# Performance work log

Hardware: AMD Instinct MI355X
Metric: run time of the kernel (lower is better)

The kernel has to match this reference:

```python
import jax, jax.numpy as jnp
import numpy as np

B, L, H, X = 64, 512, 1024, 1024
D = H + X  # 2048


def setup_inputs() -> dict:
    key = jax.random.key(0)
    k = jax.random.split(key, 8)
    h_state = jax.random.normal(k[0], (B, L, H), dtype=jnp.float32)
    x = jax.random.normal(k[1], (B, L, X), dtype=jnp.float32)
    trigger = jax.random.randint(k[2], (B, 1), 0, L, dtype=jnp.int64)
    mask = jax.random.randint(k[3], (B, L), 0, 2, dtype=jnp.int32)
    # Linear params (torch Linear: y = x @ W.T + b)
    sa = 1.0 / np.sqrt(D)
    ss = 1.0 / np.sqrt(H)
    W_a = jax.random.uniform(k[4], (D, D), jnp.float32, -sa, sa)
    b_a = jax.random.uniform(k[5], (D,), jnp.float32, -sa, sa)
    W_s = jax.random.uniform(k[6], (D, H), jnp.float32, -ss, ss)
    b_s = jax.random.uniform(k[7], (D,), jnp.float32, -ss, ss)
    return {"h_state": h_state, "x": x, "W_a": W_a, "b_a": b_a,
            "W_s": W_s, "b_s": b_s, "trigger": trigger, "mask": mask}


def reference(h_state, x, W_a, b_a, W_s, b_s, trigger, mask):
    # a: [B, L, D]
    a = jnp.concatenate((h_state, x), axis=-1)
    # direct gather of the trigger position (replaces one_hot+masked_select)
    trig_a = jnp.take_along_axis(a, trigger[:, :, None], axis=1)  # [B, 1, D]
    s = h_state.sum(axis=1)  # [B, H]
    et = jnp.tanh(jnp.einsum('bld,ed->ble', a, W_a) + b_a
                  + (s @ W_s.T + b_s)[:, None, :])  # [B, L, D]
    et = jnp.where(mask[:, :, None] == 0, jnp.float32(-1e9), et)
    attn = jax.nn.softmax(et, axis=-1)  # softmax over feature dim D (as in source)
    # dropout is identity in eval mode
    out = (trig_a * attn).sum(axis=1)  # [B, D]
    return out
```

## Files before the change

### kernel.cpp

```cpp
#include <hip/hip_runtime.h>
#include <cstdint>

#define B_ 64
#define L_ 512
#define H_ 1024
#define D_ 2048

typedef __attribute__((ext_vector_type(8))) short short8;
typedef __attribute__((ext_vector_type(4))) float f32x4;
typedef unsigned int u32;

static __device__ __forceinline__ float bf2f(u32 lo16) {
    u32 u = lo16 << 16;
    return __builtin_bit_cast(float, u);
}
static __device__ __forceinline__ unsigned short f2bf(float f) {
    u32 u = __builtin_bit_cast(u32, f);
    u += 0x7fffu + ((u >> 16) & 1u);
    return (unsigned short)(u >> 16);
}
static __device__ __forceinline__ u32 pk(float x, float y) {
    return (u32)f2bf(x) | ((u32)f2bf(y) << 16);
}
static __device__ __forceinline__ float fast_pexp(float u) {
    u = fminf(15.f, fmaxf(-15.f, u));
    float ex = __expf(2.f * u);
    float th = (ex - 1.f) / (ex + 1.f);
    return __expf(th);
}
static __device__ __forceinline__ void gload_lds16(const unsigned short* g, unsigned short* l) {
    __builtin_amdgcn_global_load_lds((const __attribute__((address_space(1))) u32*)g,
                                     (__attribute__((address_space(3))) u32*)l, 16, 0, 0);
}

__global__ __launch_bounds__(256) void k_s(const float* __restrict__ h, float* __restrict__ s) {
    int t = blockIdx.x * 256 + threadIdx.x;
    int b = t >> 10, hh = t & 1023;
    const float* p = h + ((size_t)b * L_) * H_ + hh;
    float acc = 0.f;
#pragma unroll 8
    for (int l = 0; l < L_; ++l) acc += p[(size_t)l * H_];
    s[t] = acc;
}

__global__ __launch_bounds__(256) void k_compact(const int* __restrict__ mask,
                                                 const float* __restrict__ ba,
                                                 const float* __restrict__ bs,
                                                 int* __restrict__ ridx,
                                                 int* __restrict__ cnt1,
                                                 float* __restrict__ cnt0,
                                                 float* __restrict__ t2) {
    int b = blockIdx.x;
    __shared__ int sm[L_];
    for (int l = threadIdx.x; l < L_; l += 256) sm[l] = mask[b * L_ + l];
    for (int e = threadIdx.x; e < D_; e += 256) t2[b * D_ + e] = ba[e] + bs[e];
    __syncthreads();
    if (threadIdx.x == 0) {
        int* rb = ridx + b * L_;
        int c = 0;
        for (int l = 0; l < L_; ++l) if (sm[l]) rb[c++] = l;
        int n1 = c;
        int last = (c > 0) ? rb[c - 1] : 0;
        for (; c < L_; ++c) rb[c] = last;
        cnt1[b] = n1;
        cnt0[b] = (float)(L_ - n1);
    }
}

__global__ __launch_bounds__(256) void k_cvtW(const float* __restrict__ Wa,
                                              unsigned short* __restrict__ Wb) {
    int t = blockIdx.x * 256 + threadIdx.x;
    float4 v = ((const float4*)Wa)[t];
    ((uint2*)Wb)[t] = make_uint2(pk(v.x, v.y), pk(v.z, v.w));
}

__global__ __launch_bounds__(256) void k_prep(const float* __restrict__ hs, const float* __restrict__ xx,
                                              const int* __restrict__ ridx, const int* __restrict__ cnt1,
                                              unsigned short* __restrict__ Abf) {
    int j = blockIdx.x;
    int b = blockIdx.y;
    int n1 = cnt1[b];
    if (j >= ((n1 + 127) & ~127)) return;
    int l = ridx[b * L_ + j];
    int t = threadIdx.x;
    size_t rb = ((size_t)(b * L_ + l)) << 10;
    const float* src = (t < 128) ? (hs + rb + t * 8) : (xx + rb + (t - 128) * 8);
    float4 v0 = *(const float4*)src;
    float4 v1 = *(const float4*)(src + 4);
    *(uint4*)(Abf + (((size_t)(b * L_ + j)) << 11) + t * 8) =
        make_uint4(pk(v0.x, v0.y), pk(v0.z, v0.w), pk(v1.x, v1.y), pk(v1.z, v1.w));
}

__global__ __launch_bounds__(256) void k_t2(const float* __restrict__ s, const float* __restrict__ Ws,
                                            float* __restrict__ t2) {
    __shared__ float As[16][64];
    __shared__ float Bs[16][64];
    int n0 = blockIdx.x * 64;
    int ks0 = blockIdx.y * 256;
    int tid = threadIdx.x;
    int tx = tid & 15, ty = tid >> 4;
    int r = tid >> 2, q = tid & 3;
    float acc[4][4] = {};
    for (int k0 = ks0; k0 < ks0 + 256; k0 += 16) {
        float4 av = *(const float4*)(s + (size_t)r * H_ + k0 + q * 4);
        float4 bv = *(const float4*)(Ws + (size_t)(n0 + r) * H_ + k0 + q * 4);
        __syncthreads();
        As[q*4+0][r] = av.x; As[q*4+1][r] = av.y; As[q*4+2][r] = av.z; As[q*4+3][r] = av.w;
        Bs[q*4+0][r] = bv.x; Bs[q*4+1][r] = bv.y; Bs[q*4+2][r] = bv.z; Bs[q*4+3][r] = bv.w;
        __syncthreads();
#pragma unroll
        for (int kk = 0; kk < 16; ++kk) {
            float a_[4], b_[4];
            *(float4*)&a_[0] = *(const float4*)&As[kk][ty * 4];
            *(float4*)&b_[0] = *(const float4*)&Bs[kk][tx * 4];
#pragma unroll
            for (int i = 0; i < 4; ++i)
#pragma unroll
                for (int j = 0; j < 4; ++j) acc[i][j] += a_[i] * b_[j];
        }
    }
#pragma unroll
    for (int i = 0; i < 4; ++i)
#pragma unroll
        for (int j = 0; j < 4; ++j)
            atomicAdd(&t2[(size_t)(ty * 4 + i) * D_ + n0 + tx * 4 + j], acc[i][j]);
}

#define BM 128
#define BN 128
#define BK 32

__global__ __launch_bounds__(256) void k_gemm2(
    const unsigned short* __restrict__ Abf, const unsigned short* __restrict__ Wb,
    const float* __restrict__ t2, const int* __restrict__ cnt1,
    float* __restrict__ rowsum, unsigned short* __restrict__ P)
{
    __shared__ unsigned short Asl[BM * BK];
    __shared__ unsigned short Bsl[BN * BK];
    __shared__ float red[BM];

    int tid = threadIdx.x;
    int lane = tid & 63;
    int w = tid >> 6;
    int wm = w & 1, wn = w >> 1;

    int n0 = blockIdx.x * BN;
    int jt = blockIdx.y;
    int b = jt >> 2;
    int j0 = (jt & 3) * BM;
    int n1 = cnt1[b];
    if (j0 >= n1) return;

    const unsigned short* ga = Abf + (((size_t)(b * L_ + j0 + w * 32 + (lane >> 2))) << 11) + (lane & 3) * 8;
    const unsigned short* gb = Wb  + (((size_t)(n0 + w * 32 + (lane >> 2))) << 11) + (lane & 3) * 8;
    unsigned short* la = &Asl[w * 1024];
    unsigned short* lb = &Bsl[w * 1024];

    int cl = lane & 15, kb = (lane >> 4) * 8;
    f32x4 acc[4][4] = {};

    for (int k0 = 0; k0 < D_; k0 += BK) {
        __syncthreads();
        gload_lds16(ga + k0,         la);
        gload_lds16(ga + 32768 + k0, la + 512);
        gload_lds16(gb + k0,         lb);
        gload_lds16(gb + 32768 + k0, lb + 512);
        __syncthreads();
        short8 af[4], bfg[4];
#pragma unroll
        for (int i = 0; i < 4; ++i) af[i]  = *(const short8*)&Asl[(wm*64 + i*16 + cl) * BK + kb];
#pragma unroll
        for (int j = 0; j < 4; ++j) bfg[j] = *(const short8*)&Bsl[(wn*64 + j*16 + cl) * BK + kb];
#pragma unroll
        for (int i = 0; i < 4; ++i)
#pragma unroll
            for (int j = 0; j < 4; ++j)
                acc[i][j] = __builtin_amdgcn_mfma_f32_16x16x32_bf16(af[i], bfg[j], acc[i][j], 0, 0, 0);
    }

    int qd = lane >> 4;
    float t2v[4]; int ecol[4];
#pragma unroll
    for (int j = 0; j < 4; ++j) { ecol[j] = n0 + wn*64 + j*16 + cl; t2v[j] = t2[b * D_ + ecol[j]]; }
    int orow0 = b * L_ + j0;

    float rs[4][4] = {};
#pragma unroll
    for (int i = 0; i < 4; ++i) {
        int lrowb = wm*64 + i*16 + qd*4;
#pragma unroll
        for (int j = 0; j < 4; ++j) {
#pragma unroll
            for (int g = 0; g < 4; ++g) {
                float p = fast_pexp(acc[i][j][g] + t2v[j]);
                rs[i][g] += p;
                P[(size_t)(orow0 + lrowb + g) * D_ + ecol[j]] = f2bf(p);
            }
        }
    }
#pragma unroll
    for (int i = 0; i < 4; ++i)
#pragma unroll
        for (int g = 0; g < 4; ++g) {
            float v = rs[i][g];
            v += __shfl_xor(v, 1); v += __shfl_xor(v, 2);
            v += __shfl_xor(v, 4); v += __shfl_xor(v, 8);
            rs[i][g] = v;
        }
    __syncthreads();
    if (tid < BM) red[tid] = 0.f;
    __syncthreads();
    if (cl == 0) {
#pragma unroll
        for (int i = 0; i < 4; ++i)
#pragma unroll
            for (int g = 0; g < 4; ++g)
                atomicAdd(&red[wm*64 + i*16 + qd*4 + g], rs[i][g]);
    }
    __syncthreads();
    if (tid < BM) atomicAdd(&rowsum[orow0 + tid], red[tid]);
}

__global__ __launch_bounds__(256) void k_fin2(const unsigned short* __restrict__ P,
                                              const float* __restrict__ rowsum,
                                              const int* __restrict__ cnt1,
                                              const int* __restrict__ trigger,
                                              const float* __restrict__ hs,
                                              const float* __restrict__ xx,
                                              float* __restrict__ out) {
    int b = blockIdx.y;
    __shared__ float iv[L_];
    int n1 = cnt1[b];
    int lceil = (n1 + 127) & ~127;
    for (int j = threadIdx.x; j < L_; j += 256)
        iv[j] = (j < n1) ? 1.f / rowsum[b * L_ + j] : 0.f;
    __syncthreads();
    int e0 = blockIdx.x * 512 + threadIdx.x * 2;
    const unsigned short* Pb = P + (((size_t)b) << 20) + e0;
    float s0 = 0.f, s1 = 0.f;
#pragma unroll 8
    for (int l = 0; l < lceil; ++l) {
        float f = iv[l];
        u32 pv = *(const u32*)(Pb + (((size_t)l) << 11));
        s0 += f * bf2f(pv & 0xffffu);
        s1 += f * bf2f(pv >> 16);
    }
    float base = (float)(L_ - n1) * (1.f / 2048.f);
    int trig = trigger[b];
    size_t tb = ((size_t)(b * L_ + trig)) << 10;
    float ta0 = (e0 < 1024) ? hs[tb + e0] : xx[tb + e0 - 1024];
    float ta1 = (e0 + 1 < 1024) ? hs[tb + e0 + 1] : xx[tb + e0 + 1 - 1024];
    out[b * D_ + e0]     = (s0 + base) * ta0;
    out[b * D_ + e0 + 1] = (s1 + base) * ta1;
}

#define LDK 40
__global__ __launch_bounds__(256) void k_gemm(
    const float* __restrict__ hs, const float* __restrict__ xx,
    const float* __restrict__ Wa, const unsigned short* __restrict__ Wb,
    const float* __restrict__ t2,
    const int* __restrict__ ridx, const int* __restrict__ cnt1,
    float* __restrict__ rowsum,
    unsigned short* __restrict__ P, float* __restrict__ out, int mode)
{
    __shared__ unsigned short Asl[BM][LDK];
    __shared__ unsigned short Bsl[BN][BK];
    __shared__ float red[BM];

    int tid = threadIdx.x;
    int lane = tid & 63;
    int w = tid >> 6;
    int wm = w & 1, wn = w >> 1;

    int n0 = blockIdx.x * BN;
    int jt = blockIdx.y;
    int b = jt >> 2;
    int j0 = (jt & 3) * BM;
    int n1 = cnt1[b];
    if (j0 >= n1) return;

    int r = tid >> 1;
    int koff = (tid & 1) * 16;
    int l = ridx[b * L_ + j0 + r];
    size_t abase = ((size_t)b * L_ + l) * (size_t)H_;
    const float* hrow = hs + abase;
    const float* xrow = xx + abase;
    const float* browf = Wa + (size_t)(n0 + r) * D_;
    const unsigned short* bw0 = Wb ? Wb + (size_t)(n0 + (tid >> 2)) * D_ + (tid & 3) * 8 : nullptr;
    const unsigned short* bw1 = Wb ? Wb + (size_t)(n0 + 64 + (tid >> 2)) * D_ + (tid & 3) * 8 : nullptr;
    unsigned short* bs0 = &Bsl[0][0] + (size_t)tid * 8;
    unsigned short* bs1 = &Bsl[0][0] + (size_t)(tid + 256) * 8;
    bool useWb = (Wb != nullptr);

    f32x4 acc[4][4] = {};

    for (int k0 = 0; k0 < D_; k0 += BK) {
        int k = k0 + koff;
        const float* ap = (k < H_) ? (hrow + k) : (xrow + (k - H_));
        float4 a0 = *(const float4*)(ap);
        float4 a1 = *(const float4*)(ap + 4);
        float4 a2 = *(const float4*)(ap + 8);
        float4 a3 = *(const float4*)(ap + 12);
        uint4 bv0, bv1;
        float4 c0, c1, c2, c3;
        if (useWb) {
            bv0 = *(const uint4*)(bw0 + k0);
            bv1 = *(const uint4*)(bw1 + k0);
        } else {
            const float* bp = browf + k;
            c0 = *(const float4*)(bp);
            c1 = *(const float4*)(bp + 4);
            c2 = *(const float4*)(bp + 8);
            c3 = *(const float4*)(bp + 12);
        }
        __syncthreads();
        *(uint4*)&Asl[r][koff]     = make_uint4(pk(a0.x,a0.y), pk(a0.z,a0.w), pk(a1.x,a1.y), pk(a1.z,a1.w));
        *(uint4*)&Asl[r][koff + 8] = make_uint4(pk(a2.x,a2.y), pk(a2.z,a2.w), pk(a3.x,a3.y), pk(a3.z,a3.w));
        if (useWb) {
            *(uint4*)bs0 = bv0;
            *(uint4*)bs1 = bv1;
        } else {
            *(uint4*)&Bsl[r][koff]     = make_uint4(pk(c0.x,c0.y), pk(c0.z,c0.w), pk(c1.x,c1.y), pk(c1.z,c1.w));
            *(uint4*)&Bsl[r][koff + 8] = make_uint4(pk(c2.x,c2.y), pk(c2.z,c2.w), pk(c3.x,c3.y), pk(c3.z,c3.w));
        }
        __syncthreads();
        int kb = (lane >> 4) * 8;
        short8 af[4], bfg[4];
#pragma unroll
        for (int i = 0; i < 4; ++i) af[i]  = *(const short8*)&Asl[wm*64 + i*16 + (lane & 15)][kb];
#pragma unroll
        for (int j = 0; j < 4; ++j) bfg[j] = *(const short8*)&Bsl[wn*64 + j*16 + (lane & 15)][kb];
#pragma unroll
        for (int i = 0; i < 4; ++i)
#pragma unroll
            for (int j = 0; j < 4; ++j)
                acc[i][j] = __builtin_amdgcn_mfma_f32_16x16x32_bf16(af[i], bfg[j], acc[i][j], 0, 0, 0);
    }

    int cl = lane & 15, qd = lane >> 4;
    float t2v[4]; int ecol[4];
#pragma unroll
    for (int j = 0; j < 4; ++j) { ecol[j] = n0 + wn*64 + j*16 + cl; t2v[j] = t2[b * D_ + ecol[j]]; }
    int orow0 = b * L_ + j0;

    if (mode <= 1) {
        float rs[4][4] = {};
#pragma unroll
        for (int i = 0; i < 4; ++i) {
            int lrowb = wm*64 + i*16 + qd*4;
#pragma unroll
            for (int j = 0; j < 4; ++j) {
#pragma unroll
                for (int g = 0; g < 4; ++g) {
                    float p = fast_pexp(acc[i][j][g] + t2v[j]);
                    rs[i][g] += p;
                    if (mode == 0)
                        P[(size_t)(orow0 + lrowb + g) * D_ + ecol[j]] = f2bf(p);
                }
            }
        }
#pragma unroll
        for (int i = 0; i < 4; ++i)
#pragma unroll
            for (int g = 0; g < 4; ++g) {
                float v = rs[i][g];
                v += __shfl_xor(v, 1); v += __shfl_xor(v, 2);
                v += __shfl_xor(v, 4); v += __shfl_xor(v, 8);
                rs[i][g] = v;
            }
        __syncthreads();
        if (tid < BM) red[tid] = 0.f;
        __syncthreads();
        if (cl == 0) {
#pragma unroll
            for (int i = 0; i < 4; ++i)
#pragma unroll
                for (int g = 0; g < 4; ++g)
                    atomicAdd(&red[wm*64 + i*16 + qd*4 + g], rs[i][g]);
        }
        __syncthreads();
        if (tid < BM) atomicAdd(&rowsum[orow0 + tid], red[tid]);
    } else {
        float inv[4][4];
#pragma unroll
        for (int i = 0; i < 4; ++i)
#pragma unroll
            for (int g = 0; g < 4; ++g) {
                int lrow = wm*64 + i*16 + qd*4 + g;
                inv[i][g] = (j0 + lrow < n1) ? (1.f / rowsum[orow0 + lrow]) : 0.f;
            }
        float cs[4] = {};
#pragma unroll
        for (int i = 0; i < 4; ++i)
#pragma unroll
            for (int j = 0; j < 4; ++j)
#pragma unroll
                for (int g = 0; g < 4; ++g)
                    cs[j] += fast_pexp(acc[i][j][g] + t2v[j]) * inv[i][g];
#pragma unroll
        for (int j = 0; j < 4; ++j) {
            float v = cs[j];
            v += __shfl_xor(v, 16); v += __shfl_xor(v, 32);
            cs[j] = v;
        }
        __syncthreads();
        if (tid < BN) red[tid] = 0.f;
        __syncthreads();
        if (qd == 0) {
#pragma unroll
            for (int j = 0; j < 4; ++j) atomicAdd(&red[wn*64 + j*16 + cl], cs[j]);
        }
        __syncthreads();
        if (tid < BN) atomicAdd(&out[b * D_ + n0 + tid], red[tid]);
    }
}

__global__ __launch_bounds__(256) void k_inv(const int* __restrict__ cnt1,
                                             const float* __restrict__ rowsum,
                                             float* __restrict__ invr) {
    int t = blockIdx.x * 256 + threadIdx.x;
    int b = t >> 9, j = t & 511;
    invr[t] = (j < cnt1[b]) ? (1.f / rowsum[t]) : 0.f;
}

__global__ __launch_bounds__(256) void k_fin(const unsigned short* __restrict__ P,
                                             const float* __restrict__ invr,
                                             const int* __restrict__ cnt1,
                                             float* __restrict__ out) {
    int b = blockIdx.y;
    int lz = blockIdx.z * 128;
    if (lz >= cnt1[b]) return;
    int e0 = blockIdx.x * 512 + threadIdx.x * 2;
    const unsigned short* Pb = P + ((size_t)b * L_ + lz) * D_ + e0;
    const float* ivb = invr + b * L_ + lz;
    float s0 = 0.f, s1 = 0.f;
    for (int l = 0; l < 128; ++l) {
        float iv = ivb[l];
        u32 pv = *(const u32*)(Pb + (size_t)l * D_);
        s0 += iv * bf2f(pv & 0xffffu);
        s1 += iv * bf2f(pv >> 16);
    }
    atomicAdd(&out[b * D_ + e0], s0);
    atomicAdd(&out[b * D_ + e0 + 1], s1);
}

__global__ __launch_bounds__(256) void k_final(
    const float* __restrict__ hs, const float* __restrict__ xx,
    const int* __restrict__ trigger, const float* __restrict__ cnt0,
    float* __restrict__ out) {
    int t = blockIdx.x * 256 + threadIdx.x;
    int b = t >> 11, e = t & 2047;
    int trig = trigger[b];
    size_t base = ((size_t)b * L_ + trig) * 1024;
    float ta = (e < 1024) ? hs[base + e] : xx[base + e - 1024];
    out[t] = (out[t] + cnt0[b] * (1.0f / 2048.0f)) * ta;
}

extern "C" void kernel_launch(void* const* d_in, const int* in_sizes, int n_in,
                              void* d_out, int out_size, void* d_ws, size_t ws_size,
                              hipStream_t stream) {
    const float* hs = (const float*)d_in[0];
    const float* xx = (const float*)d_in[1];
    const float* Wa = (const float*)d_in[2];
    const float* ba = (const float*)d_in[3];
    const float* Ws = (const float*)d_in[4];
    const float* bs = (const float*)d_in[5];
    const int*   trig = (const int*)d_in[6];
    const int*   mask = (const int*)d_in[7];
    float* out = (float*)d_out;

    float* wsf    = (float*)d_ws;
    float* s      = wsf;
    float* t2     = s + 65536;
    float* cnt0   = t2 + 131072;
    float* rowsum = cnt0 + 64;
    float* invr   = rowsum + 32768;
    int*   cnt1   = (int*)(invr + 32768);
    int*   ridx   = cnt1 + 64;
    unsigned short* P   = (unsigned short*)(ridx + 32768);
    unsigned short* Wb  = P + (size_t)B_ * L_ * D_;
    unsigned short* Abf = Wb + (size_t)D_ * D_;

    const size_t BASE_B   = 1180160ull;
    const size_t NEED_P   = BASE_B + 134217728ull;
    const size_t NEED_WB  = NEED_P + 8388608ull;
    const size_t NEED_ALL = NEED_WB + 134217728ull;
    bool haveP   = ws_size >= NEED_P;
    bool haveWb  = ws_size >= NEED_WB;
    bool haveAll = ws_size >= NEED_ALL;

    (void)hipMemsetAsync(rowsum, 0, (size_t)B_ * L_ * sizeof(float), stream);

    k_s      <<<256, 256, 0, stream>>>(hs, s);
    k_compact<<<B_, 256, 0, stream>>>(mask, ba, bs, ridx, cnt1, cnt0, t2);
    k_t2     <<<dim3(32, 4), 256, 0, stream>>>(s, Ws, t2);

    dim3 grid(D_ / BN, (B_ * L_) / BM);

    if (haveAll) {
        k_cvtW <<<4096, 256, 0, stream>>>(Wa, Wb);
        k_prep <<<dim3(512, 64), 256, 0, stream>>>(hs, xx, ridx, cnt1, Abf);
        k_gemm2<<<grid, 256, 0, stream>>>(Abf, Wb, t2, cnt1, rowsum, P);
        k_fin2 <<<dim3(4, 64), 256, 0, stream>>>(P, rowsum, cnt1, trig, hs, xx, out);
    } else {
        const unsigned short* WbArg = haveWb ? Wb : nullptr;
        if (haveWb) k_cvtW<<<4096, 256, 0, stream>>>(Wa, Wb);
        (void)hipMemsetAsync(out, 0, (size_t)B_ * D_ * sizeof(float), stream);
        if (haveP) {
            k_gemm<<<grid, 256, 0, stream>>>(hs, xx, Wa, WbArg, t2, ridx, cnt1, rowsum, P, out, 0);
            k_inv <<<(B_ * L_) / 256, 256, 0, stream>>>(cnt1, rowsum, invr);
            k_fin <<<dim3(4, 64, 4), 256, 0, stream>>>(P, invr, cnt1, out);
        } else {
            k_gemm<<<grid, 256, 0, stream>>>(hs, xx, Wa, WbArg, t2, ridx, cnt1, rowsum, P, out, 1);
            k_gemm<<<grid, 256, 0, stream>>>(hs, xx, Wa, WbArg, t2, ridx, cnt1, rowsum, P, out, 2);
        }
        k_final<<<(B_ * D_) / 256, 256, 0, stream>>>(hs, xx, trig, cnt0, out);
    }
}
```

Before: 680.2 us.

## Replace bf16 GEMM with 256x256-tile, 8-wave, double-buffered LDS pipelined kernel

Replaces the 128x128 single-buffered MFMA GEMM with a 256x256 tile kernel using 512 threads, a 64-wide K step and double-buffered LDS (128 KB). Global-to-LDS loads for the next K tiles are interleaved with four MFMA phases, using barriers and s_setprio to overlap memory traffic with matrix compute and to raise reuse per loaded byte. Row padding in the prep kernel moves to multiples of 256 to match the larger M tile. The larger tile wastes more work on partially masked batches and its heavy LDS and register use limits occupancy.

```diff
diff --git a/kernel.cpp b/kernel.cpp
--- a/kernel.cpp
+++ b/kernel.cpp
@@ -80,7 +80,7 @@
     int j = blockIdx.x;
     int b = blockIdx.y;
     int n1 = cnt1[b];
-    if (j >= ((n1 + 127) & ~127)) return;
+    if (j >= ((n1 + 255) & ~255)) return;
     int l = ridx[b * L_ + j];
     int t = threadIdx.x;
     size_t rb = ((size_t)(b * L_ + l)) << 10;
@@ -126,99 +126,183 @@
             atomicAdd(&t2[(size_t)(ty * 4 + i) * D_ + n0 + tx * 4 + j], acc[i][j]);
 }
 
-#define BM 128
-#define BN 128
-#define BK 32
-
-__global__ __launch_bounds__(256) void k_gemm2(
+#define BAR3() do { asm volatile("" ::: "memory"); __builtin_amdgcn_s_barrier(); asm volatile("" ::: "memory"); } while (0)
+
+__global__ __launch_bounds__(512, 2) void k_gemm3(
     const unsigned short* __restrict__ Abf, const unsigned short* __restrict__ Wb,
     const float* __restrict__ t2, const int* __restrict__ cnt1,
     float* __restrict__ rowsum, unsigned short* __restrict__ P)
 {
-    __shared__ unsigned short Asl[BM * BK];
-    __shared__ unsigned short Bsl[BN * BK];
-    __shared__ float red[BM];
+    __shared__ unsigned short lds[65536];
 
     int tid = threadIdx.x;
     int lane = tid & 63;
     int w = tid >> 6;
-    int wm = w & 1, wn = w >> 1;
-
-    int n0 = blockIdx.x * BN;
+    int wm = w >> 2;
+    int wn = w & 3;
+    int g = lane >> 4;
+    int cl = lane & 15;
+
+    int n0 = blockIdx.x * 256;
     int jt = blockIdx.y;
-    int b = jt >> 2;
-    int j0 = (jt & 3) * BM;
+    int b = jt >> 1;
+    int j0 = (jt & 1) * 256;
     int n1 = cnt1[b];
     if (j0 >= n1) return;
 
-    const unsigned short* ga = Abf + (((size_t)(b * L_ + j0 + w * 32 + (lane >> 2))) << 11) + (lane & 3) * 8;
-    const unsigned short* gb = Wb  + (((size_t)(n0 + w * 32 + (lane >> 2))) << 11) + (lane & 3) * 8;
-    unsigned short* la = &Asl[w * 1024];
-    unsigned short* lb = &Bsl[w * 1024];
-
-    int cl = lane & 15, kb = (lane >> 4) * 8;
-    f32x4 acc[4][4] = {};
-
-    for (int k0 = 0; k0 < D_; k0 += BK) {
-        __syncthreads();
-        gload_lds16(ga + k0,         la);
-        gload_lds16(ga + 32768 + k0, la + 512);
-        gload_lds16(gb + k0,         lb);
-        gload_lds16(gb + 32768 + k0, lb + 512);
-        __syncthreads();
-        short8 af[4], bfg[4];
-#pragma unroll
-        for (int i = 0; i < 4; ++i) af[i]  = *(const short8*)&Asl[(wm*64 + i*16 + cl) * BK + kb];
-#pragma unroll
-        for (int j = 0; j < 4; ++j) bfg[j] = *(const short8*)&Bsl[(wn*64 + j*16 + cl) * BK + kb];
-#pragma unroll
-        for (int i = 0; i < 4; ++i)
-#pragma unroll
-            for (int j = 0; j < 4; ++j)
-                acc[i][j] = __builtin_amdgcn_mfma_f32_16x16x32_bf16(af[i], bfg[j], acc[i][j], 0, 0, 0);
-    }
-
-    int qd = lane >> 4;
+    int sr = tid >> 2;
+    int sce = (tid & 3) * 8;
+    const unsigned short* aS0 = Abf + (((size_t)(b * L_ + j0 + sr)) << 11) + sce;
+    const unsigned short* aS1 = aS0 + ((size_t)128 << 11);
+    const unsigned short* bS0 = Wb + (((size_t)(n0 + sr)) << 11) + sce;
+    const unsigned short* bS1 = bS0 + ((size_t)128 << 11);
+    int wq = w * 512;
+
+#define STAGE_A3(h, tk, u) do { \
+        const unsigned short* s_ = ((h) ? aS1 : aS0) + (tk) * 64; \
+        unsigned short* d_ = &lds[(u) * 32768 + (h) * 8192 + wq]; \
+        gload_lds16(s_, d_); gload_lds16(s_ + 32, d_ + 4096); } while (0)
+#define STAGE_B3(h, tk, u) do { \
+        const unsigned short* s_ = ((h) ? bS1 : bS0) + (tk) * 64; \
+        unsigned short* d_ = &lds[(u) * 32768 + 16384 + (h) * 8192 + wq]; \
+        gload_lds16(s_, d_); gload_lds16(s_ + 32, d_ + 4096); } while (0)
+
+    int rdA = wm * 8192 + cl * 32 + g * 8;
+    int rdB = 16384 + (wn >> 1) * 8192 + ((wn & 1) * 64 + cl) * 32 + g * 8;
+
+    f32x4 acc[8][4] = {};
+    short8 af[4][2], bf0[2][2], bf1[2][2];
+
+    STAGE_A3(0, 0, 0); STAGE_B3(0, 0, 0); STAGE_B3(1, 0, 0); STAGE_A3(1, 0, 0);
+    STAGE_B3(0, 1, 1); STAGE_B3(1, 1, 1); STAGE_A3(0, 1, 1);
+    asm volatile("s_waitcnt vmcnt(6)" ::: "memory");
+    BAR3();
+
+    for (int t = 0; t < 32; ++t) {
+        int u = t & 1;
+        int ub = u * 32768;
+        int tn = (t + 1) & 31, tnn = (t + 2) & 31;
+
+#pragma unroll
+        for (int m = 0; m < 4; ++m) {
+            af[m][0] = *(const short8*)&lds[ub + rdA + m * 512];
+            af[m][1] = *(const short8*)&lds[ub + rdA + 4096 + m * 512];
+        }
+#pragma unroll
+        for (int n = 0; n < 2; ++n) {
+            bf0[n][0] = *(const short8*)&lds[ub + rdB + n * 512];
+            bf0[n][1] = *(const short8*)&lds[ub + rdB + 4096 + n * 512];
+        }
+        STAGE_A3(1, tn, u ^ 1);
+        BAR3();
+        __builtin_amdgcn_s_setprio(1);
+#pragma unroll
+        for (int m = 0; m < 4; ++m)
+#pragma unroll
+            for (int n = 0; n < 2; ++n) {
+                acc[m][n] = __builtin_amdgcn_mfma_f32_16x16x32_bf16(af[m][0], bf0[n][0], acc[m][n], 0, 0, 0);
+                acc[m][n] = __builtin_amdgcn_mfma_f32_16x16x32_bf16(af[m][1], bf0[n][1], acc[m][n], 0, 0, 0);
+            }
+        __builtin_amdgcn_s_setprio(0);
+        BAR3();
+
+#pragma unroll
+        for (int n = 0; n < 2; ++n) {
+            bf1[n][0] = *(const short8*)&lds[ub + rdB + (n + 2) * 512];
+            bf1[n][1] = *(const short8*)&lds[ub + rdB + 4096 + (n + 2) * 512];
+        }
+        BAR3();
+        __builtin_amdgcn_s_setprio(1);
+#pragma unroll
+        for (int m = 0; m < 4; ++m)
+#pragma unroll
+            for (int n = 0; n < 2; ++n) {
+                acc[m][n + 2] = __builtin_amdgcn_mfma_f32_16x16x32_bf16(af[m][0], bf1[n][0], acc[m][n + 2], 0, 0, 0);
+                acc[m][n + 2] = __builtin_amdgcn_mfma_f32_16x16x32_bf16(af[m][1], bf1[n][1], acc[m][n + 2], 0, 0, 0);
+            }
+        __builtin_amdgcn_s_setprio(0);
+        BAR3();
+
+#pragma unroll
+        for (int m = 0; m < 4; ++m) {
+            af[m][0] = *(const short8*)&lds[ub + rdA + (m + 4) * 512];
+            af[m][1] = *(const short8*)&lds[ub + rdA + 4096 + (m + 4) * 512];
+        }
+        STAGE_B3(0, tnn, u);
+        BAR3();
+        __builtin_amdgcn_s_setprio(1);
+#pragma unroll
+        for (int m = 0; m < 4; ++m)
+#pragma unroll
+            for (int n = 0; n < 2; ++n) {
+                acc[m + 4][n + 2] = __builtin_amdgcn_mfma_f32_16x16x32_bf16(af[m][0], bf1[n][0], acc[m + 4][n + 2], 0, 0, 0);
+                acc[m + 4][n + 2] = __builtin_amdgcn_mfma_f32_16x16x32_bf16(af[m][1], bf1[n][1], acc[m + 4][n + 2], 0, 0, 0);
+            }
+        __builtin_amdgcn_s_setprio(0);
+        BAR3();
+
+        STAGE_B3(1, tnn, u);
+        STAGE_A3(0, tnn, u);
+        asm volatile("s_waitcnt vmcnt(6)" ::: "memory");
+        BAR3();
+        __builtin_amdgcn_s_setprio(1);
+#pragma unroll
+        for (int m = 0; m < 4; ++m)
+#pragma unroll
+            for (int n = 0; n < 2; ++n) {
+                acc[m + 4][n] = __builtin_amdgcn_mfma_f32_16x16x32_bf16(af[m][0], bf0[n][0], acc[m + 4][n], 0, 0, 0);
+                acc[m + 4][n] = __builtin_amdgcn_mfma_f32_16x16x32_bf16(af[m][1], bf0[n][1], acc[m + 4][n], 0, 0, 0);
+            }
+        __builtin_amdgcn_s_setprio(0);
+        BAR3();
+    }
+#undef STAGE_A3
+#undef STAGE_B3
+
+    asm volatile("s_waitcnt vmcnt(0)" ::: "memory");
+    __syncthreads();
+
     float t2v[4]; int ecol[4];
 #pragma unroll
-    for (int j = 0; j < 4; ++j) { ecol[j] = n0 + wn*64 + j*16 + cl; t2v[j] = t2[b * D_ + ecol[j]]; }
-    int orow0 = b * L_ + j0;
-
-    float rs[4][4] = {};
-#pragma unroll
-    for (int i = 0; i < 4; ++i) {
-        int lrowb = wm*64 + i*16 + qd*4;
-#pragma unroll
-        for (int j = 0; j < 4; ++j) {
-#pragma unroll
-            for (int g = 0; g < 4; ++g) {
-                float p = fast_pexp(acc[i][j][g] + t2v[j]);
-                rs[i][g] += p;
-                P[(size_t)(orow0 + lrowb + g) * D_ + ecol[j]] = f2bf(p);
-            }
-        }
-    }
-#pragma unroll
-    for (int i = 0; i < 4; ++i)
-#pragma unroll
-        for (int g = 0; g < 4; ++g) {
-            float v = rs[i][g];
+    for (int n = 0; n < 4; ++n) { ecol[n] = n0 + wn * 64 + n * 16 + cl; t2v[n] = t2[b * D_ + ecol[n]]; }
+    int orow0 = b * L_ + j0 + wm * 128;
+    int qd = g;
+
+    float rs[8][4] = {};
+#pragma unroll
+    for (int m = 0; m < 8; ++m) {
+        int lrowb = m * 16 + qd * 4;
+#pragma unroll
+        for (int n = 0; n < 4; ++n) {
+#pragma unroll
+            for (int gg = 0; gg < 4; ++gg) {
+                float p = fast_pexp(acc[m][n][gg] + t2v[n]);
+                rs[m][gg] += p;
+                P[(size_t)(orow0 + lrowb + gg) * D_ + ecol[n]] = f2bf(p);
+            }
+        }
+    }
+#pragma unroll
+    for (int m = 0; m < 8; ++m)
+#pragma unroll
+        for (int gg = 0; gg < 4; ++gg) {
+            float v = rs[m][gg];
             v += __shfl_xor(v, 1); v += __shfl_xor(v, 2);
             v += __shfl_xor(v, 4); v += __shfl_xor(v, 8);
-            rs[i][g] = v;
-        }
-    __syncthreads();
-    if (tid < BM) red[tid] = 0.f;
+            rs[m][gg] = v;
+        }
+    float* red = (float*)lds;
+    if (tid < 256) red[tid] = 0.f;
     __syncthreads();
     if (cl == 0) {
 #pragma unroll
-        for (int i = 0; i < 4; ++i)
-#pragma unroll
-            for (int g = 0; g < 4; ++g)
-                atomicAdd(&red[wm*64 + i*16 + qd*4 + g], rs[i][g]);
+        for (int m = 0; m < 8; ++m)
+#pragma unroll
+            for (int gg = 0; gg < 4; ++gg)
+                atomicAdd(&red[wm * 128 + m * 16 + qd * 4 + gg], rs[m][gg]);
     }
     __syncthreads();
-    if (tid < BM) atomicAdd(&rowsum[orow0 + tid], red[tid]);
+    if (tid < 256) atomicAdd(&rowsum[b * L_ + j0 + tid], red[tid]);
 }
 
 __global__ __launch_bounds__(256) void k_fin2(const unsigned short* __restrict__ P,
@@ -254,6 +338,9 @@
     out[b * D_ + e0 + 1] = (s1 + base) * ta1;
 }
 
+#define BM 128
+#define BN 128
+#define BK 32
 #define LDK 40
 __global__ __launch_bounds__(256) void k_gemm(
     const float* __restrict__ hs, const float* __restrict__ xx,
@@ -495,14 +582,13 @@
     k_compact<<<B_, 256, 0, stream>>>(mask, ba, bs, ridx, cnt1, cnt0, t2);
     k_t2     <<<dim3(32, 4), 256, 0, stream>>>(s, Ws, t2);
 
-    dim3 grid(D_ / BN, (B_ * L_) / BM);
-
     if (haveAll) {
         k_cvtW <<<4096, 256, 0, stream>>>(Wa, Wb);
         k_prep <<<dim3(512, 64), 256, 0, stream>>>(hs, xx, ridx, cnt1, Abf);
-        k_gemm2<<<grid, 256, 0, stream>>>(Abf, Wb, t2, cnt1, rowsum, P);
+        k_gemm3<<<dim3(8, 128), 512, 0, stream>>>(Abf, Wb, t2, cnt1, rowsum, P);
         k_fin2 <<<dim3(4, 64), 256, 0, stream>>>(P, rowsum, cnt1, trig, hs, xx, out);
     } else {
+        dim3 grid(D_ / BN, (B_ * L_) / BM);
         const unsigned short* WbArg = haveWb ? Wb : nullptr;
         if (haveWb) k_cvtW<<<4096, 256, 0, stream>>>(Wa, Wb);
         (void)hipMemsetAsync(out, 0, (size_t)B_ * D_ * sizeof(float), stream);
```

After: 719.2 us. +5.7%, slower.
